# Kernel tuning notes

Measured on AMD Instinct MI355X. Metric: run time of the kernel, lower is better.

## Reference

```python
import jax, jax.numpy as jnp
import numpy as np

D_MODEL = 14
N_HEADS = 2
SINK_TEMP = 0.1
SINK_ITERS = 20
EPS = 1e-10


def setup_inputs() -> dict:
    key = jax.random.key(0)
    ks = jax.random.split(key, 12)
    b, n, d = 64, 1024, D_MODEL
    s = 1.0 / np.sqrt(d)
    return {
        "x": jax.random.normal(ks[0], (b, n, d), dtype=jnp.float32),
        "certainty": jax.random.uniform(ks[1], (b, n), dtype=jnp.float32),
        "permutation": jax.random.randint(ks[2], (b, n), 0, n).astype(jnp.int64),
        "Wq": jax.random.normal(ks[3], (d, d), dtype=jnp.float32) * s,
        "bq": jnp.zeros((d,), dtype=jnp.float32),
        "Wk": jax.random.normal(ks[4], (d, d), dtype=jnp.float32) * s,
        "bk": jnp.zeros((d,), dtype=jnp.float32),
        "Wv": jax.random.normal(ks[5], (d, d), dtype=jnp.float32) * s,
        "bv": jnp.zeros((d,), dtype=jnp.float32),
        "Wo": jax.random.normal(ks[6], (d, d), dtype=jnp.float32) * s,
        "bo": jnp.zeros((d,), dtype=jnp.float32),
    }


def _split_heads(t, b, n):
    # (b, n, d) -> (b, H, n, hd)
    return t.reshape(b, n, N_HEADS, D_MODEL // N_HEADS).transpose(0, 2, 1, 3)


def reference(x, certainty, permutation, Wq, bq, Wk, bk, Wv, bv, Wo, bo):
    b, n, d = x.shape
    hd = d // N_HEADS
    Q = _split_heads(x @ Wq.T + bq, b, n)
    K = _split_heads(x @ Wk.T + bk, b, n)
    V = _split_heads(x @ Wv.T + bv, b, n)
    scores = jnp.einsum("bhqd,bhkd->bhqk", Q, K) / jnp.sqrt(jnp.float32(hd))
    attn = jax.nn.softmax(scores, axis=-1)  # dropout is identity at eval
    out = jnp.einsum("bhqk,bhkd->bhqd", attn, V)
    out = out.transpose(0, 2, 1, 3).reshape(b, n, d)
    out = out @ Wo.T + bo

    avg_attn = attn.mean(axis=1)  # (b, n, n)
    entropy = -jnp.sum(avg_attn * jnp.log(avg_attn + EPS), axis=-1)  # (b, n)
    max_entropy = jnp.log(jnp.float32(n))
    cert_update = jax.nn.sigmoid(max_entropy - entropy)
    new_certainty = jnp.maximum(certainty, cert_update)

    logits = jnp.log(avg_attn + EPS)
    P = jnp.exp(logits / SINK_TEMP)

    def body(_, P):
        P = P / (P.sum(axis=-1, keepdims=True) + EPS)
        P = P / (P.sum(axis=-2, keepdims=True) + EPS)
        return P

    P = jax.lax.fori_loop(0, SINK_ITERS, body, P)
    new_perm = jnp.argmax(P, axis=-1)  # (b, n)
    new_permutation = jnp.take_along_axis(permutation, new_perm, axis=1)
    return out, new_certainty, new_permutation
```

## Files before the change

### kernel.cpp

```cpp
#include <hip/hip_runtime.h>

#define EPSF    1e-10f
#define MAXENT  6.93147180559945286f
#define SCALEF  0.37796447300922720f

__device__ __forceinline__ float wave_sum(float v) {
#pragma unroll
  for (int off = 32; off > 0; off >>= 1) v += __shfl_xor(v, off);
  return v;
}
__device__ __forceinline__ void wave_sum2(float& a, float& b) {
#pragma unroll
  for (int off = 32; off > 0; off >>= 1) {
    a += __shfl_xor(a, off);
    b += __shfl_xor(b, off);
  }
}
__device__ __forceinline__ void fma4(float a, float4 b, float4& c) {
  c.x = fmaf(a, b.x, c.x); c.y = fmaf(a, b.y, c.y);
  c.z = fmaf(a, b.z, c.z); c.w = fmaf(a, b.w, c.w);
}
__device__ __forceinline__ float dot4(float4 a, float4 b, float acc) {
  acc = fmaf(a.x, b.x, acc); acc = fmaf(a.y, b.y, acc);
  acc = fmaf(a.z, b.z, acc); acc = fmaf(a.w, b.w, acc);
  return acc;
}
__device__ __forceinline__ float exp4sum(float4 s) {
  return __expf(s.x) + __expf(s.y) + __expf(s.z) + __expf(s.w);
}
__device__ __forceinline__ float p0e(float s1, float s2, float E1, float E2) {
  float p = fmaf(E1, __expf(s1), fmaf(E2, __expf(s2), EPSF));
  float p2 = p * p, p4 = p2 * p2, p5 = p4 * p;
  return p5 * p5;
}

__global__ __launch_bounds__(256) void qkv_kernel(
    const float* __restrict__ x,
    const float* __restrict__ Wq, const float* __restrict__ bq,
    const float* __restrict__ Wk, const float* __restrict__ bk,
    const float* __restrict__ Wv, const float* __restrict__ bv,
    float* __restrict__ Qt, float* __restrict__ Kt, float* __restrict__ Vt,
    float* __restrict__ R, float* __restrict__ CA, float* __restrict__ CB) {
  int row = blockIdx.x * 256 + threadIdx.x;
  int b = row >> 10, i = row & 1023;
  float xv[14];
#pragma unroll
  for (int k = 0; k < 14; k++) xv[k] = x[row * 14 + k];
#pragma unroll
  for (int d = 0; d < 14; d++) {
    float q = bq[d], kk = bk[d], vv = bv[d];
#pragma unroll
    for (int k = 0; k < 14; k++) {
      q  = fmaf(xv[k], Wq[d * 14 + k], q);
      kk = fmaf(xv[k], Wk[d * 14 + k], kk);
      vv = fmaf(xv[k], Wv[d * 14 + k], vv);
    }
    int o = b * 14336 + d * 1024 + i;
    Qt[o] = q * SCALEF;
    Kt[o] = kk; Vt[o] = vv;
  }
  R[row] = 1.0f;
  CA[row] = 1.0f;
  CB[row] = 1.0f;
}

__global__ __launch_bounds__(512) void attn_kernel(
    const float* __restrict__ Qt, const float* __restrict__ Kt, const float* __restrict__ Vt,
    const float* __restrict__ cert_in,
    float* __restrict__ E1o, float* __restrict__ E2o,
    float* __restrict__ attn_o, float* __restrict__ cert_out) {
  __shared__ float4 Kl[3584];
  int b = blockIdx.x >> 6;
  int rg = blockIdx.x & 63;
  int tid = threadIdx.x;
  const float4* Ktb = (const float4*)(Kt + b * 14336);
  for (int idx = tid; idx < 3584; idx += 512) Kl[idx] = Ktb[idx];
  __syncthreads();

  int wave = tid >> 6, lane = tid & 63;
  int i0 = rg * 16 + wave * 2;
  float q0[14], q1[14];
#pragma unroll
  for (int d = 0; d < 14; d++) {
    q0[d] = Qt[b * 14336 + d * 1024 + i0];
    q1[d] = Qt[b * 14336 + d * 1024 + i0 + 1];
  }

  float L10 = 0.f, L20 = 0.f, L11 = 0.f, L21 = 0.f;
#pragma unroll
  for (int t = 0; t < 4; t++) {
    int g = t * 64 + lane;
    float4 kv[7];
#pragma unroll
    for (int d = 0; d < 7; d++) kv[d] = Kl[d * 256 + g];
    float4 sa = {0,0,0,0}, sb = {0,0,0,0};
#pragma unroll
    for (int d = 0; d < 7; d++) { fma4(q0[d], kv[d], sa); fma4(q1[d], kv[d], sb); }
    L10 += exp4sum(sa); L11 += exp4sum(sb);
#pragma unroll
    for (int d = 0; d < 7; d++) kv[d] = Kl[(d + 7) * 256 + g];
    sa = make_float4(0,0,0,0); sb = make_float4(0,0,0,0);
#pragma unroll
    for (int d = 0; d < 7; d++) { fma4(q0[d + 7], kv[d], sa); fma4(q1[d + 7], kv[d], sb); }
    L20 += exp4sum(sa); L21 += exp4sum(sb);
  }
  L10 = wave_sum(L10); L20 = wave_sum(L20);
  L11 = wave_sum(L11); L21 = wave_sum(L21);
  float i10 = 1.0f / L10, i20 = 1.0f / L20, i11 = 1.0f / L11, i21 = 1.0f / L21;

  float acc0[14], acc1[14];
#pragma unroll
  for (int d = 0; d < 14; d++) { acc0[d] = 0.f; acc1[d] = 0.f; }
  float ent0 = 0.f, ent1 = 0.f;
  const float4* Vtb = (const float4*)(Vt + b * 14336);
#pragma unroll
  for (int t = 0; t < 4; t++) {
    int g = t * 64 + lane;
    float4 kv[7];
#pragma unroll
    for (int d = 0; d < 7; d++) kv[d] = Kl[d * 256 + g];
    float4 sa = {0,0,0,0}, sb = {0,0,0,0};
#pragma unroll
    for (int d = 0; d < 7; d++) { fma4(q0[d], kv[d], sa); fma4(q1[d], kv[d], sb); }
    float4 e10 = make_float4(__expf(sa.x), __expf(sa.y), __expf(sa.z), __expf(sa.w));
    float4 e11 = make_float4(__expf(sb.x), __expf(sb.y), __expf(sb.z), __expf(sb.w));
#pragma unroll
    for (int d = 0; d < 7; d++) kv[d] = Kl[(d + 7) * 256 + g];
    sa = make_float4(0,0,0,0); sb = make_float4(0,0,0,0);
#pragma unroll
    for (int d = 0; d < 7; d++) { fma4(q0[d + 7], kv[d], sa); fma4(q1[d + 7], kv[d], sb); }
    float4 e20 = make_float4(__expf(sa.x), __expf(sa.y), __expf(sa.z), __expf(sa.w));
    float4 e21 = make_float4(__expf(sb.x), __expf(sb.y), __expf(sb.z), __expf(sb.w));
#pragma unroll
    for (int d = 0; d < 7; d++) {
      float4 vv = Vtb[d * 256 + g];
      acc0[d] += e10.x * vv.x + e10.y * vv.y + e10.z * vv.z + e10.w * vv.w;
      acc1[d] += e11.x * vv.x + e11.y * vv.y + e11.z * vv.z + e11.w * vv.w;
    }
#pragma unroll
    for (int d = 7; d < 14; d++) {
      float4 vv = Vtb[d * 256 + g];
      acc0[d] += e20.x * vv.x + e20.y * vv.y + e20.z * vv.z + e20.w * vv.w;
      acc1[d] += e21.x * vv.x + e21.y * vv.y + e21.z * vv.z + e21.w * vv.w;
    }
    float a;
    a = 0.5f * (e10.x * i10 + e20.x * i20); ent0 -= a * __logf(a + EPSF);
    a = 0.5f * (e10.y * i10 + e20.y * i20); ent0 -= a * __logf(a + EPSF);
    a = 0.5f * (e10.z * i10 + e20.z * i20); ent0 -= a * __logf(a + EPSF);
    a = 0.5f * (e10.w * i10 + e20.w * i20); ent0 -= a * __logf(a + EPSF);
    a = 0.5f * (e11.x * i11 + e21.x * i21); ent1 -= a * __logf(a + EPSF);
    a = 0.5f * (e11.y * i11 + e21.y * i21); ent1 -= a * __logf(a + EPSF);
    a = 0.5f * (e11.z * i11 + e21.z * i21); ent1 -= a * __logf(a + EPSF);
    a = 0.5f * (e11.w * i11 + e21.w * i21); ent1 -= a * __logf(a + EPSF);
  }
  ent0 = wave_sum(ent0); ent1 = wave_sum(ent1);
#pragma unroll
  for (int d = 0; d < 14; d++) { acc0[d] = wave_sum(acc0[d]); acc1[d] = wave_sum(acc1[d]); }

  if (lane == 0) {
    int row0 = b * 1024 + i0;
    E1o[row0] = 0.5f * i10;  E2o[row0] = 0.5f * i20;
    E1o[row0 + 1] = 0.5f * i11; E2o[row0 + 1] = 0.5f * i21;
#pragma unroll
    for (int d = 0; d < 14; d++) {
      attn_o[row0 * 14 + d] = acc0[d] * (d < 7 ? i10 : i20);
      attn_o[(row0 + 1) * 14 + d] = acc1[d] * (d < 7 ? i11 : i21);
    }
    cert_out[row0] = fmaxf(cert_in[row0], 1.0f / (1.0f + __expf(ent0 - MAXENT)));
    cert_out[row0 + 1] = fmaxf(cert_in[row0 + 1], 1.0f / (1.0f + __expf(ent1 - MAXENT)));
  }
}

__global__ __launch_bounds__(256) void proj_kernel(
    const float* __restrict__ attn_o, const float* __restrict__ Wo,
    const float* __restrict__ bo, float* __restrict__ out) {
  int idx = blockIdx.x * 256 + threadIdx.x;
  if (idx >= 917504) return;
  int row = idx / 14, d = idx - row * 14;
  float s = bo[d];
  const float* ar = attn_o + row * 14;
  const float* wr = Wo + d * 14;
#pragma unroll
  for (int k = 0; k < 14; k++) s = fmaf(ar[k], wr[k], s);
  out[idx] = s;
}


__global__ __launch_bounds__(512) void p0pre_kernel(
    const float* __restrict__ Qt, const float* __restrict__ Kt,
    const float* __restrict__ E1, const float* __restrict__ E2,
    float* __restrict__ P0, int b0) {
  __shared__ float4 Kl[3584];
  int gb = blockIdx.x >> 5, blk = blockIdx.x & 31;
  int b = b0 + gb;
  int tid = threadIdx.x;
  const float4* Ktb = (const float4*)(Kt + b * 14336);
  for (int idx = tid; idx < 3584; idx += 512) Kl[idx] = Ktb[idx];
  __syncthreads();

  int wave = tid >> 6, lane = tid & 63;
  int i0 = blk * 32 + wave * 4;
  float q[4][14], e1r[4], e2r[4];
#pragma unroll
  for (int rr = 0; rr < 4; rr++) {
#pragma unroll
    for (int d = 0; d < 14; d++) q[rr][d] = Qt[b * 14336 + d * 1024 + i0 + rr];
    e1r[rr] = E1[b * 1024 + i0 + rr];
    e2r[rr] = E2[b * 1024 + i0 + rr];
  }
  float4* P0f4 = (float4*)P0;
#pragma unroll
  for (int t = 0; t < 4; t++) {
    int g = t * 64 + lane;
    float4 kv[14];
#pragma unroll
    for (int d = 0; d < 14; d++) kv[d] = Kl[d * 256 + g];
#pragma unroll
    for (int rr = 0; rr < 4; rr++) {
      float4 s1 = {0,0,0,0}, s2 = {0,0,0,0};
#pragma unroll
      for (int d = 0; d < 7; d++)  fma4(q[rr][d], kv[d], s1);
#pragma unroll
      for (int d = 7; d < 14; d++) fma4(q[rr][d], kv[d], s2);
      float4 pv;
      pv.x = p0e(s1.x, s2.x, e1r[rr], e2r[rr]);
      pv.y = p0e(s1.y, s2.y, e1r[rr], e2r[rr]);
      pv.z = p0e(s1.z, s2.z, e1r[rr], e2r[rr]);
      pv.w = p0e(s1.w, s2.w, e1r[rr], e2r[rr]);
      P0f4[(size_t)(gb * 1024 + i0 + rr) * 256 + g] = pv;
    }
  }
}

#define SINK_LOGS 4
#define SINK_S    16
__global__ __launch_bounds__(512) void sink_fused(
    const float* __restrict__ P0, const float* __restrict__ Cin,
    float* __restrict__ Cout, float* __restrict__ R,
    const float* __restrict__ vprev, float* __restrict__ vcur,
    int b0, int G) {
  __shared__ float Cl[1024];
  __shared__ float vbuf[8192];
  int tid = threadIdx.x;
  int gb = blockIdx.x >> SINK_LOGS, slice = blockIdx.x & (SINK_S - 1);
  int b = b0 + gb;

  for (int col = tid; col < 1024; col += 512) {
    float cv = Cin[b * 1024 + col];
    if (vprev) {
      const float* vp = vprev + gb * 1024 + col;
      float v = 0.f;
#pragma unroll
      for (int s = 0; s < SINK_S; s++) v += vp[(size_t)s * G * 1024];
      cv = fminf(cv / fmaf(cv, v, EPSF), 1e37f);
      if (slice == 0) Cout[b * 1024 + col] = cv;
    }
    Cl[col] = cv;
  }
  __syncthreads();

  int wave = tid >> 6, lane = tid & 63;
  int i0 = slice * 64 + wave * 8;
  int rbase = b * 1024 + i0;
  int l0 = lane, l1 = 64 + lane, l2 = 128 + lane, l3 = 192 + lane;
  const float4* Cl4 = (const float4*)Cl;
  float4 c0 = Cl4[l0], c1 = Cl4[l1], c2 = Cl4[l2], c3 = Cl4[l3];
  float4 v0 = {0,0,0,0}, v1 = {0,0,0,0}, v2 = {0,0,0,0}, v3 = {0,0,0,0};
  const float4* base = (const float4*)P0 + (size_t)(gb * 1024 + i0) * 256;

  float rreg[8];
#pragma unroll
  for (int r = 0; r < 8; r++) rreg[r] = R[rbase + r];

  float4 a0 = base[l0], a1 = base[l1], a2 = base[l2], a3 = base[l3];
  float4 b0f = base[256 + l0], b1f = base[256 + l1], b2f = base[256 + l2], b3f = base[256 + l3];

#pragma unroll
  for (int r = 0; r < 8; r += 2) {
    float4 na0, na1, na2, na3, nb0, nb1, nb2, nb3;
    if (r + 2 < 8) {
      const float4* nxt = base + (r + 2) * 256;
      na0 = nxt[l0]; na1 = nxt[l1]; na2 = nxt[l2]; na3 = nxt[l3];
      nb0 = nxt[256 + l0]; nb1 = nxt[256 + l1]; nb2 = nxt[256 + l2]; nb3 = nxt[256 + l3];
    }
    float ua = dot4(a3, c3, dot4(a2, c2, dot4(a1, c1, dot4(a0, c0, 0.f))));
    float ub = dot4(b3f, c3, dot4(b2f, c2, dot4(b1f, c1, dot4(b0f, c0, 0.f))));
    wave_sum2(ua, ub);
    float rva = rreg[r], rvb = rreg[r + 1];
    rva = fminf(rva / fmaf(rva, ua, EPSF), 1e37f);
    rvb = fminf(rvb / fmaf(rvb, ub, EPSF), 1e37f);
    if (lane == 0) { R[rbase + r] = rva; R[rbase + r + 1] = rvb; }
    fma4(rva, a0, v0); fma4(rva, a1, v1); fma4(rva, a2, v2); fma4(rva, a3, v3);
    fma4(rvb, b0f, v0); fma4(rvb, b1f, v1); fma4(rvb, b2f, v2); fma4(rvb, b3f, v3);
    if (r + 2 < 8) {
      a0 = na0; a1 = na1; a2 = na2; a3 = na3;
      b0f = nb0; b1f = nb1; b2f = nb2; b3f = nb3;
    }
  }
  float4* vb4 = (float4*)vbuf;
  vb4[wave * 256 + l0] = v0; vb4[wave * 256 + l1] = v1;
  vb4[wave * 256 + l2] = v2; vb4[wave * 256 + l3] = v3;
  __syncthreads();
  for (int col = tid; col < 1024; col += 512) {
    float v = 0.f;
#pragma unroll
    for (int w = 0; w < 8; w++) v += vbuf[w * 1024 + col];
    vcur[(size_t)(slice * G + gb) * 1024 + col] = v;
  }
}

__global__ __launch_bounds__(256) void cfinal_kernel(
    const float* __restrict__ Cin, float* __restrict__ Cfin,
    const float* __restrict__ vprev, int b0, int G) {
  int idx = blockIdx.x * 256 + threadIdx.x;
  int gb = idx >> 10, col = idx & 1023;
  const float* vp = vprev + gb * 1024 + col;
  float v = 0.f;
#pragma unroll
  for (int s = 0; s < SINK_S; s++) v += vp[(size_t)s * G * 1024];
  int o = (b0 + gb) * 1024 + col;
  float cv = Cin[o];
  Cfin[o] = fminf(cv / fmaf(cv, v, EPSF), 1e37f);
}

__global__ __launch_bounds__(512) void argmaxP_kernel(
    const float* __restrict__ P0, const float* __restrict__ Cg,
    const int* __restrict__ perm, float* __restrict__ perm_out, int b0) {
  int gb = blockIdx.x >> 7, rg = blockIdx.x & 127;
  int b = b0 + gb;
  int tid = threadIdx.x;
  int wave = tid >> 6, lane = tid & 63;
  int i = rg * 8 + wave;
  const float4* Cb = (const float4*)(Cg + b * 1024);
  const float4* Prow = (const float4*)P0 + (size_t)(gb * 1024 + i) * 256;

  float best = -1.0f;
  int bj = 0;
#pragma unroll
  for (int t = 0; t < 4; t++) {
    int g = t * 64 + lane;
    float4 pv = Prow[g], cv = Cb[g];
    float val;
    val = pv.x * cv.x; if (val > best) { best = val; bj = 4 * g + 0; }
    val = pv.y * cv.y; if (val > best) { best = val; bj = 4 * g + 1; }
    val = pv.z * cv.z; if (val > best) { best = val; bj = 4 * g + 2; }
    val = pv.w * cv.w; if (val > best) { best = val; bj = 4 * g + 3; }
  }
#pragma unroll
  for (int off = 32; off > 0; off >>= 1) {
    float ob = __shfl_xor(best, off);
    int oj = __shfl_xor(bj, off);
    if (ob > best || (ob == best && oj < bj)) { best = ob; bj = oj; }
  }
  if (lane == 0) perm_out[b * 1024 + i] = (float)perm[b * 1024 + bj];
}


__global__ __launch_bounds__(512) void sinkA_kernel(
    const float* __restrict__ Qt, const float* __restrict__ Kt,
    const float* __restrict__ E1, const float* __restrict__ E2,
    const float* __restrict__ C, float* __restrict__ R) {
  __shared__ float4 Kl[3584];
  int b = blockIdx.x >> 5, blk = blockIdx.x & 31;
  int tid = threadIdx.x;
  const float4* Ktb = (const float4*)(Kt + b * 14336);
  for (int idx = tid; idx < 3584; idx += 512) Kl[idx] = Ktb[idx];
  __syncthreads();
  int wave = tid >> 6, lane = tid & 63;
  int i0 = blk * 32 + wave * 4;
  float q[4][14], e1r[4], e2r[4], u[4];
#pragma unroll
  for (int rr = 0; rr < 4; rr++) {
#pragma unroll
    for (int d = 0; d < 14; d++) q[rr][d] = Qt[b * 14336 + d * 1024 + i0 + rr];
    e1r[rr] = E1[b * 1024 + i0 + rr];
    e2r[rr] = E2[b * 1024 + i0 + rr];
    u[rr] = 0.f;
  }
  const float4* Cb = (const float4*)(C + b * 1024);
#pragma unroll
  for (int t = 0; t < 4; t++) {
    int g = t * 64 + lane;
    float4 kv[14];
#pragma unroll
    for (int d = 0; d < 14; d++) kv[d] = Kl[d * 256 + g];
    float4 cv = Cb[g];
#pragma unroll
    for (int rr = 0; rr < 4; rr++) {
      float4 s1 = {0,0,0,0}, s2 = {0,0,0,0};
#pragma unroll
      for (int d = 0; d < 7; d++)  fma4(q[rr][d], kv[d], s1);
#pragma unroll
      for (int d = 7; d < 14; d++) fma4(q[rr][d], kv[d], s2);
      u[rr] += p0e(s1.x, s2.x, e1r[rr], e2r[rr]) * cv.x;
      u[rr] += p0e(s1.y, s2.y, e1r[rr], e2r[rr]) * cv.y;
      u[rr] += p0e(s1.z, s2.z, e1r[rr], e2r[rr]) * cv.z;
      u[rr] += p0e(s1.w, s2.w, e1r[rr], e2r[rr]) * cv.w;
    }
  }
#pragma unroll
  for (int rr = 0; rr < 4; rr++) u[rr] = wave_sum(u[rr]);
  if (lane == 0) {
#pragma unroll
    for (int rr = 0; rr < 4; rr++) {
      int o = b * 1024 + i0 + rr;
      float rv = R[o];
      R[o] = fminf(rv / fmaf(rv, u[rr], EPSF), 1e37f);
    }
  }
}

__global__ __launch_bounds__(512) void sinkB_kernel(
    const float* __restrict__ Qt, const float* __restrict__ Kt,
    const float* __restrict__ E1, const float* __restrict__ E2,
    const float* __restrict__ R, float* __restrict__ C) {
  __shared__ float4 Ql[3584];
  int b = blockIdx.x >> 5, blk = blockIdx.x & 31;
  int tid = threadIdx.x;
  const float4* Qtb = (const float4*)(Qt + b * 14336);
  for (int idx = tid; idx < 3584; idx += 512) Ql[idx] = Qtb[idx];
  __syncthreads();
  int wave = tid >> 6, lane = tid & 63;
  int j0 = blk * 32 + wave * 4;
  float kk[4][14], v[4];
#pragma unroll
  for (int rr = 0; rr < 4; rr++) {
#pragma unroll
    for (int d = 0; d < 14; d++) kk[rr][d] = Kt[b * 14336 + d * 1024 + j0 + rr];
    v[rr] = 0.f;
  }
  const float4* E1b = (const float4*)(E1 + b * 1024);
  const float4* E2b = (const float4*)(E2 + b * 1024);
  const float4* Rb  = (const float4*)(R + b * 1024);
#pragma unroll
  for (int t = 0; t < 4; t++) {
    int g = t * 64 + lane;
    float4 qv[14];
#pragma unroll
    for (int d = 0; d < 14; d++) qv[d] = Ql[d * 256 + g];
    float4 e1v = E1b[g], e2v = E2b[g], rv = Rb[g];
#pragma unroll
    for (int rr = 0; rr < 4; rr++) {
      float4 s1 = {0,0,0,0}, s2 = {0,0,0,0};
#pragma unroll
      for (int d = 0; d < 7; d++)  fma4(kk[rr][d], qv[d], s1);
#pragma unroll
      for (int d = 7; d < 14; d++) fma4(kk[rr][d], qv[d], s2);
      v[rr] += p0e(s1.x, s2.x, e1v.x, e2v.x) * rv.x;
      v[rr] += p0e(s1.y, s2.y, e1v.y, e2v.y) * rv.y;
      v[rr] += p0e(s1.z, s2.z, e1v.z, e2v.z) * rv.z;
      v[rr] += p0e(s1.w, s2.w, e1v.w, e2v.w) * rv.w;
    }
  }
#pragma unroll
  for (int rr = 0; rr < 4; rr++) v[rr] = wave_sum(v[rr]);
  if (lane == 0) {
#pragma unroll
    for (int rr = 0; rr < 4; rr++) {
      int o = b * 1024 + j0 + rr;
      float cv = C[o];
      C[o] = fminf(cv / fmaf(cv, v[rr], EPSF), 1e37f);
    }
  }
}

__global__ __launch_bounds__(512) void argmax_kernel(
    const float* __restrict__ Qt, const float* __restrict__ Kt,
    const float* __restrict__ E1, const float* __restrict__ E2,
    const float* __restrict__ C, const int* __restrict__ perm,
    float* __restrict__ perm_out) {
  __shared__ float4 Kl[3584];
  int b = blockIdx.x >> 7, rg = blockIdx.x & 127;
  int tid = threadIdx.x;
  const float4* Ktb = (const float4*)(Kt + b * 14336);
  for (int idx = tid; idx < 3584; idx += 512) Kl[idx] = Ktb[idx];
  __syncthreads();
  int wave = tid >> 6, lane = tid & 63;
  int i = rg * 8 + wave;
  int row = b * 1024 + i;
  float q[14];
#pragma unroll
  for (int d = 0; d < 14; d++) q[d] = Qt[b * 14336 + d * 1024 + i];
  float e1r = E1[row], e2r = E2[row];
  const float4* Cb = (const float4*)(C + b * 1024);
  float best = -1.0f;
  int bj = 0;
#pragma unroll
  for (int t = 0; t < 4; t++) {
    int g = t * 64 + lane;
    float4 kv[14];
#pragma unroll
    for (int d = 0; d < 14; d++) kv[d] = Kl[d * 256 + g];
    float4 cv = Cb[g];
    float4 s1 = {0,0,0,0}, s2 = {0,0,0,0};
#pragma unroll
    for (int d = 0; d < 7; d++)  fma4(q[d], kv[d], s1);
#pragma unroll
    for (int d = 7; d < 14; d++) fma4(q[d], kv[d], s2);
    float val;
    val = p0e(s1.x, s2.x, e1r, e2r) * cv.x; if (val > best) { best = val; bj = 4 * g + 0; }
    val = p0e(s1.y, s2.y, e1r, e2r) * cv.y; if (val > best) { best = val; bj = 4 * g + 1; }
    val = p0e(s1.z, s2.z, e1r, e2r) * cv.z; if (val > best) { best = val; bj = 4 * g + 2; }
    val = p0e(s1.w, s2.w, e1r, e2r) * cv.w; if (val > best) { best = val; bj = 4 * g + 3; }
  }
#pragma unroll
  for (int off = 32; off > 0; off >>= 1) {
    float ob = __shfl_xor(best, off);
    int oj = __shfl_xor(bj, off);
    if (ob > best || (ob == best && oj < bj)) { best = ob; bj = oj; }
  }
  if (lane == 0) perm_out[row] = (float)perm[b * 1024 + bj];
}

extern "C" void kernel_launch(void* const* d_in, const int* in_sizes, int n_in,
                              void* d_out, int out_size, void* d_ws, size_t ws_size,
                              hipStream_t stream) {
  const float* x    = (const float*)d_in[0];
  const float* cert = (const float*)d_in[1];
  const int*   perm = (const int*)d_in[2];
  const float* Wq = (const float*)d_in[3];
  const float* bq = (const float*)d_in[4];
  const float* Wk = (const float*)d_in[5];
  const float* bk = (const float*)d_in[6];
  const float* Wv = (const float*)d_in[7];
  const float* bv = (const float*)d_in[8];
  const float* Wo = (const float*)d_in[9];
  const float* bo = (const float*)d_in[10];

  float* out      = (float*)d_out;
  float* cert_out = out + 917504;
  float* perm_out = out + 983040;

  float* ws = (float*)d_ws;
  float* Qt = ws;
  float* Kt = Qt + 917504;
  float* Vt = Kt + 917504;
  float* E1 = Vt + 917504;
  float* E2 = E1 + 65536;
  float* R  = E2 + 65536;
  float* CA = R + 65536;
  float* CB = CA + 65536;
  float* attn_o = CB + 65536;
  float* vpp0   = attn_o + 917504;

  size_t base_f = 3997696u;
  size_t avail_f = (ws_size / 4 > base_f) ? (ws_size / 4 - base_f) : 0;
  int G = 0;
  if (avail_f >= (size_t)64 * (32768 + 1048576)) G = 64;
  else if (avail_f >= (size_t)32 * (32768 + 1048576)) G = 32;
  else if (avail_f >= (size_t)16 * (32768 + 1048576)) G = 16;

  float* Cbuf[2] = {CA, CB};

  qkv_kernel<<<256, 256, 0, stream>>>(x, Wq, bq, Wk, bk, Wv, bv, Qt, Kt, Vt, R, CA, CB);
  attn_kernel<<<4096, 512, 0, stream>>>(Qt, Kt, Vt, cert, E1, E2, attn_o, cert_out);
  proj_kernel<<<3584, 256, 0, stream>>>(attn_o, Wo, bo, out);

  if (G >= 16) {
    float* vpp[2] = {vpp0, vpp0 + (size_t)16 * G * 1024};
    float* P0 = vpp0 + (size_t)32 * G * 1024;
    for (int b0 = 0; b0 < 64; b0 += G) {
      p0pre_kernel<<<G * 32, 512, 0, stream>>>(Qt, Kt, E1, E2, P0, b0);
      for (int it = 1; it <= 20; it++) {
        const float* vprev = (it == 1) ? nullptr : vpp[(it - 1) & 1];
        float* vcur = vpp[it & 1];
        const float* Cin = Cbuf[it & 1];
        float* Cout = Cbuf[(it + 1) & 1];
        sink_fused<<<G * SINK_S, 512, 0, stream>>>(P0, Cin, Cout, R, vprev, vcur, b0, G);
      }
      cfinal_kernel<<<G * 4, 256, 0, stream>>>(Cbuf[1], Cbuf[0], vpp[0], b0, G);
      argmaxP_kernel<<<G * 128, 512, 0, stream>>>(P0, Cbuf[0], perm, perm_out, b0);
    }
  } else {
    for (int it = 0; it < 20; it++) {
      sinkA_kernel<<<2048, 512, 0, stream>>>(Qt, Kt, E1, E2, CA, R);
      sinkB_kernel<<<2048, 512, 0, stream>>>(Qt, Kt, E1, E2, R, CA);
    }
    argmax_kernel<<<8192, 512, 0, stream>>>(Qt, Kt, E1, E2, CA, perm, perm_out);
  }
}
```

Baseline: 1.426 ms.

## Register-block attention rows and split Sinkhorn row sweep into more slices

The attention kernel now handles four query rows per wave instead of two. Each K tile read from LDS and each V load is reused across more rows, and half as many blocks are launched. The fused Sinkhorn kernel uses 32 slices of 32 rows instead of 16 slices of 64 rows, with a launch-bounds occupancy hint, to put more blocks on this memory-bound pass. It also drops the software prefetch of the next row pair. Workspace sizing follows SINK_S. The trade-off is higher register pressure in attention and twice as many partial column-sum vectors to write and reduce in Sinkhorn.

After: 3.093 ms. 2.17x slower.

```diff
diff --git a/kernel.cpp b/kernel.cpp
--- a/kernel.cpp
+++ b/kernel.cpp
@@ -70,104 +70,122 @@
     float* __restrict__ E1o, float* __restrict__ E2o,
     float* __restrict__ attn_o, float* __restrict__ cert_out) {
   __shared__ float4 Kl[3584];
-  int b = blockIdx.x >> 6;
-  int rg = blockIdx.x & 63;
+  int b = blockIdx.x >> 5;
+  int rg = blockIdx.x & 31;
   int tid = threadIdx.x;
   const float4* Ktb = (const float4*)(Kt + b * 14336);
   for (int idx = tid; idx < 3584; idx += 512) Kl[idx] = Ktb[idx];
   __syncthreads();
 
   int wave = tid >> 6, lane = tid & 63;
-  int i0 = rg * 16 + wave * 2;
-  float q0[14], q1[14];
-#pragma unroll
-  for (int d = 0; d < 14; d++) {
-    q0[d] = Qt[b * 14336 + d * 1024 + i0];
-    q1[d] = Qt[b * 14336 + d * 1024 + i0 + 1];
-  }
-
-  float L10 = 0.f, L20 = 0.f, L11 = 0.f, L21 = 0.f;
+  int i0 = rg * 32 + wave * 4;
+  float q[4][14];
+#pragma unroll
+  for (int rr = 0; rr < 4; rr++)
+#pragma unroll
+    for (int d = 0; d < 14; d++) q[rr][d] = Qt[b * 14336 + d * 1024 + i0 + rr];
+
+  float L1[4] = {0, 0, 0, 0}, L2[4] = {0, 0, 0, 0};
 #pragma unroll
   for (int t = 0; t < 4; t++) {
     int g = t * 64 + lane;
     float4 kv[7];
 #pragma unroll
     for (int d = 0; d < 7; d++) kv[d] = Kl[d * 256 + g];
-    float4 sa = {0,0,0,0}, sb = {0,0,0,0};
-#pragma unroll
-    for (int d = 0; d < 7; d++) { fma4(q0[d], kv[d], sa); fma4(q1[d], kv[d], sb); }
-    L10 += exp4sum(sa); L11 += exp4sum(sb);
+#pragma unroll
+    for (int rr = 0; rr < 4; rr++) {
+      float4 s = {0, 0, 0, 0};
+#pragma unroll
+      for (int d = 0; d < 7; d++) fma4(q[rr][d], kv[d], s);
+      L1[rr] += exp4sum(s);
+    }
 #pragma unroll
     for (int d = 0; d < 7; d++) kv[d] = Kl[(d + 7) * 256 + g];
-    sa = make_float4(0,0,0,0); sb = make_float4(0,0,0,0);
-#pragma unroll
-    for (int d = 0; d < 7; d++) { fma4(q0[d + 7], kv[d], sa); fma4(q1[d + 7], kv[d], sb); }
-    L20 += exp4sum(sa); L21 += exp4sum(sb);
-  }
-  L10 = wave_sum(L10); L20 = wave_sum(L20);
-  L11 = wave_sum(L11); L21 = wave_sum(L21);
-  float i10 = 1.0f / L10, i20 = 1.0f / L20, i11 = 1.0f / L11, i21 = 1.0f / L21;
-
-  float acc0[14], acc1[14];
-#pragma unroll
-  for (int d = 0; d < 14; d++) { acc0[d] = 0.f; acc1[d] = 0.f; }
-  float ent0 = 0.f, ent1 = 0.f;
+#pragma unroll
+    for (int rr = 0; rr < 4; rr++) {
+      float4 s = {0, 0, 0, 0};
+#pragma unroll
+      for (int d = 0; d < 7; d++) fma4(q[rr][d + 7], kv[d], s);
+      L2[rr] += exp4sum(s);
+    }
+  }
+#pragma unroll
+  for (int rr = 0; rr < 4; rr++) wave_sum2(L1[rr], L2[rr]);
+  float i1[4], i2[4];
+#pragma unroll
+  for (int rr = 0; rr < 4; rr++) { i1[rr] = 1.0f / L1[rr]; i2[rr] = 1.0f / L2[rr]; }
+
+  float acc[4][14];
+#pragma unroll
+  for (int rr = 0; rr < 4; rr++)
+#pragma unroll
+    for (int d = 0; d < 14; d++) acc[rr][d] = 0.f;
+  float ent[4] = {0, 0, 0, 0};
   const float4* Vtb = (const float4*)(Vt + b * 14336);
 #pragma unroll
   for (int t = 0; t < 4; t++) {
     int g = t * 64 + lane;
     float4 kv[7];
+    float4 e1[4], e2[4];
 #pragma unroll
     for (int d = 0; d < 7; d++) kv[d] = Kl[d * 256 + g];
-    float4 sa = {0,0,0,0}, sb = {0,0,0,0};
-#pragma unroll
-    for (int d = 0; d < 7; d++) { fma4(q0[d], kv[d], sa); fma4(q1[d], kv[d], sb); }
-    float4 e10 = make_float4(__expf(sa.x), __expf(sa.y), __expf(sa.z), __expf(sa.w));
-    float4 e11 = make_float4(__expf(sb.x), __expf(sb.y), __expf(sb.z), __expf(sb.w));
+#pragma unroll
+    for (int rr = 0; rr < 4; rr++) {
+      float4 s = {0, 0, 0, 0};
+#pragma unroll
+      for (int d = 0; d < 7; d++) fma4(q[rr][d], kv[d], s);
+      e1[rr] = make_float4(__expf(s.x), __expf(s.y), __expf(s.z), __expf(s.w));
+    }
 #pragma unroll
     for (int d = 0; d < 7; d++) kv[d] = Kl[(d + 7) * 256 + g];
-    sa = make_float4(0,0,0,0); sb = make_float4(0,0,0,0);
-#pragma unroll
-    for (int d = 0; d < 7; d++) { fma4(q0[d + 7], kv[d], sa); fma4(q1[d + 7], kv[d], sb); }
-    float4 e20 = make_float4(__expf(sa.x), __expf(sa.y), __expf(sa.z), __expf(sa.w));
-    float4 e21 = make_float4(__expf(sb.x), __expf(sb.y), __expf(sb.z), __expf(sb.w));
+#pragma unroll
+    for (int rr = 0; rr < 4; rr++) {
+      float4 s = {0, 0, 0, 0};
+#pragma unroll
+      for (int d = 0; d < 7; d++) fma4(q[rr][d + 7], kv[d], s);
+      e2[rr] = make_float4(__expf(s.x), __expf(s.y), __expf(s.z), __expf(s.w));
+    }
 #pragma unroll
     for (int d = 0; d < 7; d++) {
       float4 vv = Vtb[d * 256 + g];
-      acc0[d] += e10.x * vv.x + e10.y * vv.y + e10.z * vv.z + e10.w * vv.w;
-      acc1[d] += e11.x * vv.x + e11.y * vv.y + e11.z * vv.z + e11.w * vv.w;
+#pragma unroll
+      for (int rr = 0; rr < 4; rr++)
+        acc[rr][d] += e1[rr].x * vv.x + e1[rr].y * vv.y + e1[rr].z * vv.z + e1[rr].w * vv.w;
     }
 #pragma unroll
     for (int d = 7; d < 14; d++) {
       float4 vv = Vtb[d * 256 + g];
-      acc0[d] += e20.x * vv.x + e20.y * vv.y + e20.z * vv.z + e20.w * vv.w;
-      acc1[d] += e21.x * vv.x + e21.y * vv.y + e21.z * vv.z + e21.w * vv.w;
-    }
-    float a;
-    a = 0.5f * (e10.x * i10 + e20.x * i20); ent0 -= a * __logf(a + EPSF);
-    a = 0.5f * (e10.y * i10 + e20.y * i20); ent0 -= a * __logf(a + EPSF);
-    a = 0.5f * (e10.z * i10 + e20.z * i20); ent0 -= a * __logf(a + EPSF);
-    a = 0.5f * (e10.w * i10 + e20.w * i20); ent0 -= a * __logf(a + EPSF);
-    a = 0.5f * (e11.x * i11 + e21.x * i21); ent1 -= a * __logf(a + EPSF);
-    a = 0.5f * (e11.y * i11 + e21.y * i21); ent1 -= a * __logf(a + EPSF);
-    a = 0.5f * (e11.z * i11 + e21.z * i21); ent1 -= a * __logf(a + EPSF);
-    a = 0.5f * (e11.w * i11 + e21.w * i21); ent1 -= a * __logf(a + EPSF);
-  }
-  ent0 = wave_sum(ent0); ent1 = wave_sum(ent1);
-#pragma unroll
-  for (int d = 0; d < 14; d++) { acc0[d] = wave_sum(acc0[d]); acc1[d] = wave_sum(acc1[d]); }
+#pragma unroll
+      for (int rr = 0; rr < 4; rr++)
+        acc[rr][d] += e2[rr].x * vv.x + e2[rr].y * vv.y + e2[rr].z * vv.z + e2[rr].w * vv.w;
+    }
+#pragma unroll
+    for (int rr = 0; rr < 4; rr++) {
+      float a;
+      a = 0.5f * (e1[rr].x * i1[rr] + e2[rr].x * i2[rr]); ent[rr] -= a * __logf(a + EPSF);
+      a = 0.5f * (e1[rr].y * i1[rr] + e2[rr].y * i2[rr]); ent[rr] -= a * __logf(a + EPSF);
+      a = 0.5f * (e1[rr].z * i1[rr] + e2[rr].z * i2[rr]); ent[rr] -= a * __logf(a + EPSF);
+      a = 0.5f * (e1[rr].w * i1[rr] + e2[rr].w * i2[rr]); ent[rr] -= a * __logf(a + EPSF);
+    }
+  }
+#pragma unroll
+  for (int rr = 0; rr < 4; rr += 2) wave_sum2(ent[rr], ent[rr + 1]);
+#pragma unroll
+  for (int rr = 0; rr < 4; rr++)
+#pragma unroll
+    for (int d = 0; d < 14; d += 2) wave_sum2(acc[rr][d], acc[rr][d + 1]);
 
   if (lane == 0) {
-    int row0 = b * 1024 + i0;
-    E1o[row0] = 0.5f * i10;  E2o[row0] = 0.5f * i20;
-    E1o[row0 + 1] = 0.5f * i11; E2o[row0 + 1] = 0.5f * i21;
-#pragma unroll
-    for (int d = 0; d < 14; d++) {
-      attn_o[row0 * 14 + d] = acc0[d] * (d < 7 ? i10 : i20);
-      attn_o[(row0 + 1) * 14 + d] = acc1[d] * (d < 7 ? i11 : i21);
-    }
-    cert_out[row0] = fmaxf(cert_in[row0], 1.0f / (1.0f + __expf(ent0 - MAXENT)));
-    cert_out[row0 + 1] = fmaxf(cert_in[row0 + 1], 1.0f / (1.0f + __expf(ent1 - MAXENT)));
+#pragma unroll
+    for (int rr = 0; rr < 4; rr++) {
+      int row = b * 1024 + i0 + rr;
+      E1o[row] = 0.5f * i1[rr];
+      E2o[row] = 0.5f * i2[rr];
+#pragma unroll
+      for (int d = 0; d < 14; d++)
+        attn_o[row * 14 + d] = acc[rr][d] * (d < 7 ? i1[rr] : i2[rr]);
+      cert_out[row] = fmaxf(cert_in[row], 1.0f / (1.0f + __expf(ent[rr] - MAXENT)));
+    }
   }
 }
 
@@ -232,9 +250,9 @@
   }
 }
 
-#define SINK_LOGS 4
-#define SINK_S    16
-__global__ __launch_bounds__(512) void sink_fused(
+#define SINK_LOGS 5
+#define SINK_S    32
+__global__ __launch_bounds__(512, 6) void sink_fused(
     const float* __restrict__ P0, const float* __restrict__ Cin,
     float* __restrict__ Cout, float* __restrict__ R,
     const float* __restrict__ vprev, float* __restrict__ vcur,
@@ -260,7 +278,7 @@
   __syncthreads();
 
   int wave = tid >> 6, lane = tid & 63;
-  int i0 = slice * 64 + wave * 8;
+  int i0 = slice * 32 + wave * 4;
   int rbase = b * 1024 + i0;
   int l0 = lane, l1 = 64 + lane, l2 = 128 + lane, l3 = 192 + lane;
   const float4* Cl4 = (const float4*)Cl;
@@ -268,21 +286,16 @@
   float4 v0 = {0,0,0,0}, v1 = {0,0,0,0}, v2 = {0,0,0,0}, v3 = {0,0,0,0};
   const float4* base = (const float4*)P0 + (size_t)(gb * 1024 + i0) * 256;
 
-  float rreg[8];
-#pragma unroll
-  for (int r = 0; r < 8; r++) rreg[r] = R[rbase + r];
-
-  float4 a0 = base[l0], a1 = base[l1], a2 = base[l2], a3 = base[l3];
-  float4 b0f = base[256 + l0], b1f = base[256 + l1], b2f = base[256 + l2], b3f = base[256 + l3];
-
-#pragma unroll
-  for (int r = 0; r < 8; r += 2) {
-    float4 na0, na1, na2, na3, nb0, nb1, nb2, nb3;
-    if (r + 2 < 8) {
-      const float4* nxt = base + (r + 2) * 256;
-      na0 = nxt[l0]; na1 = nxt[l1]; na2 = nxt[l2]; na3 = nxt[l3];
-      nb0 = nxt[256 + l0]; nb1 = nxt[256 + l1]; nb2 = nxt[256 + l2]; nb3 = nxt[256 + l3];
-    }
+  float rreg[4];
+#pragma unroll
+  for (int r = 0; r < 4; r++) rreg[r] = R[rbase + r];
+
+#pragma unroll
+  for (int r = 0; r < 4; r += 2) {
+    const float4* rowA = base + r * 256;
+    const float4* rowB = rowA + 256;
+    float4 a0 = rowA[l0], a1 = rowA[l1], a2 = rowA[l2], a3 = rowA[l3];
+    float4 b0f = rowB[l0], b1f = rowB[l1], b2f = rowB[l2], b3f = rowB[l3];
     float ua = dot4(a3, c3, dot4(a2, c2, dot4(a1, c1, dot4(a0, c0, 0.f))));
     float ub = dot4(b3f, c3, dot4(b2f, c2, dot4(b1f, c1, dot4(b0f, c0, 0.f))));
     wave_sum2(ua, ub);
@@ -292,10 +305,6 @@
     if (lane == 0) { R[rbase + r] = rva; R[rbase + r + 1] = rvb; }
     fma4(rva, a0, v0); fma4(rva, a1, v1); fma4(rva, a2, v2); fma4(rva, a3, v3);
     fma4(rvb, b0f, v0); fma4(rvb, b1f, v1); fma4(rvb, b2f, v2); fma4(rvb, b3f, v3);
-    if (r + 2 < 8) {
-      a0 = na0; a1 = na1; a2 = na2; a3 = na3;
-      b0f = nb0; b1f = nb1; b2f = nb2; b3f = nb3;
-    }
   }
   float4* vb4 = (float4*)vbuf;
   vb4[wave * 256 + l0] = v0; vb4[wave * 256 + l1] = v1;
@@ -545,20 +554,21 @@
 
   size_t base_f = 3997696u;
   size_t avail_f = (ws_size / 4 > base_f) ? (ws_size / 4 - base_f) : 0;
+  size_t perG = 2u * SINK_S * 1024 + 1048576u;
   int G = 0;
-  if (avail_f >= (size_t)64 * (32768 + 1048576)) G = 64;
-  else if (avail_f >= (size_t)32 * (32768 + 1048576)) G = 32;
-  else if (avail_f >= (size_t)16 * (32768 + 1048576)) G = 16;
+  if (avail_f >= 64 * perG) G = 64;
+  else if (avail_f >= 32 * perG) G = 32;
+  else if (avail_f >= 16 * perG) G = 16;
 
   float* Cbuf[2] = {CA, CB};
 
   qkv_kernel<<<256, 256, 0, stream>>>(x, Wq, bq, Wk, bk, Wv, bv, Qt, Kt, Vt, R, CA, CB);
-  attn_kernel<<<4096, 512, 0, stream>>>(Qt, Kt, Vt, cert, E1, E2, attn_o, cert_out);
+  attn_kernel<<<2048, 512, 0, stream>>>(Qt, Kt, Vt, cert, E1, E2, attn_o, cert_out);
   proj_kernel<<<3584, 256, 0, stream>>>(attn_o, Wo, bo, out);
 
   if (G >= 16) {
-    float* vpp[2] = {vpp0, vpp0 + (size_t)16 * G * 1024};
-    float* P0 = vpp0 + (size_t)32 * G * 1024;
+    float* vpp[2] = {vpp0, vpp0 + (size_t)SINK_S * G * 1024};
+    float* P0 = vpp0 + (size_t)2 * SINK_S * G * 1024;
     for (int b0 = 0; b0 < 64; b0 += G) {
       p0pre_kernel<<<G * 32, 512, 0, stream>>>(Qt, Kt, E1, E2, P0, b0);
       for (int it = 1; it <= 20; it++) {
```

## Fuse first Sinkhorn iteration into P0 precompute kernel

Applied to the files above, without the earlier changes.

The P0 precompute kernel now also does the first Sinkhorn row normalization and writes column partial sums, which removes one sink_fused launch and one full pass over P0. It reads back the P0 rows it just wrote (likely still in cache) to build the column partials, writing 32 partial slices instead of 16, so the next iteration's reduction reads more data. The column-scale update in sink_fused is also vectorized to float4 over 256 threads, and the workspace layout is enlarged to hold the wider partial buffers.

Result: no change. 1.426 ms (-0.0%).

```diff
diff --git a/kernel.cpp b/kernel.cpp
--- a/kernel.cpp
+++ b/kernel.cpp
@@ -186,10 +186,11 @@
 }
 
 
-__global__ __launch_bounds__(512) void p0pre_kernel(
+__global__ __launch_bounds__(512) void p0sink1_kernel(
     const float* __restrict__ Qt, const float* __restrict__ Kt,
     const float* __restrict__ E1, const float* __restrict__ E2,
-    float* __restrict__ P0, int b0) {
+    float* __restrict__ P0, float* __restrict__ R,
+    float* __restrict__ vpart, int b0, int G) {
   __shared__ float4 Kl[3584];
   int gb = blockIdx.x >> 5, blk = blockIdx.x & 31;
   int b = b0 + gb;
@@ -200,13 +201,14 @@
 
   int wave = tid >> 6, lane = tid & 63;
   int i0 = blk * 32 + wave * 4;
-  float q[4][14], e1r[4], e2r[4];
+  float q[4][14], e1r[4], e2r[4], u[4];
 #pragma unroll
   for (int rr = 0; rr < 4; rr++) {
 #pragma unroll
     for (int d = 0; d < 14; d++) q[rr][d] = Qt[b * 14336 + d * 1024 + i0 + rr];
     e1r[rr] = E1[b * 1024 + i0 + rr];
     e2r[rr] = E2[b * 1024 + i0 + rr];
+    u[rr] = 0.f;
   }
   float4* P0f4 = (float4*)P0;
 #pragma unroll
@@ -228,7 +230,40 @@
       pv.z = p0e(s1.z, s2.z, e1r[rr], e2r[rr]);
       pv.w = p0e(s1.w, s2.w, e1r[rr], e2r[rr]);
       P0f4[(size_t)(gb * 1024 + i0 + rr) * 256 + g] = pv;
-    }
+      u[rr] += pv.x; u[rr] += pv.y; u[rr] += pv.z; u[rr] += pv.w;
+    }
+  }
+  wave_sum2(u[0], u[1]); wave_sum2(u[2], u[3]);
+  float rv[4];
+#pragma unroll
+  for (int rr = 0; rr < 4; rr++) {
+    float r0 = 1.0f;
+    rv[rr] = fminf(r0 / fmaf(r0, u[rr], EPSF), 1e37f);
+  }
+  if (lane == 0) {
+#pragma unroll
+    for (int rr = 0; rr < 4; rr++) R[b * 1024 + i0 + rr] = rv[rr];
+  }
+  int l0 = lane, l1 = 64 + lane, l2 = 128 + lane, l3 = 192 + lane;
+  float4 v0 = {0,0,0,0}, v1 = {0,0,0,0}, v2 = {0,0,0,0}, v3 = {0,0,0,0};
+  const float4* base = P0f4 + (size_t)(gb * 1024 + i0) * 256;
+#pragma unroll
+  for (int rr = 0; rr < 4; rr++) {
+    const float4* row = base + rr * 256;
+    float4 a0 = row[l0], a1 = row[l1], a2 = row[l2], a3 = row[l3];
+    fma4(rv[rr], a0, v0); fma4(rv[rr], a1, v1); fma4(rv[rr], a2, v2); fma4(rv[rr], a3, v3);
+  }
+  __syncthreads();
+  float* vbuf = (float*)Kl;
+  float4* vb4 = (float4*)vbuf;
+  vb4[wave * 256 + l0] = v0; vb4[wave * 256 + l1] = v1;
+  vb4[wave * 256 + l2] = v2; vb4[wave * 256 + l3] = v3;
+  __syncthreads();
+  for (int col = tid; col < 1024; col += 512) {
+    float v = 0.f;
+#pragma unroll
+    for (int w = 0; w < 8; w++) v += vbuf[w * 1024 + col];
+    vpart[(size_t)(blk * G + gb) * 1024 + col] = v;
   }
 }
 
@@ -238,24 +273,28 @@
     const float* __restrict__ P0, const float* __restrict__ Cin,
     float* __restrict__ Cout, float* __restrict__ R,
     const float* __restrict__ vprev, float* __restrict__ vcur,
-    int b0, int G) {
+    int b0, int G, int Sprev) {
   __shared__ float Cl[1024];
   __shared__ float vbuf[8192];
   int tid = threadIdx.x;
   int gb = blockIdx.x >> SINK_LOGS, slice = blockIdx.x & (SINK_S - 1);
   int b = b0 + gb;
 
-  for (int col = tid; col < 1024; col += 512) {
-    float cv = Cin[b * 1024 + col];
-    if (vprev) {
-      const float* vp = vprev + gb * 1024 + col;
-      float v = 0.f;
-#pragma unroll
-      for (int s = 0; s < SINK_S; s++) v += vp[(size_t)s * G * 1024];
-      cv = fminf(cv / fmaf(cv, v, EPSF), 1e37f);
-      if (slice == 0) Cout[b * 1024 + col] = cv;
-    }
-    Cl[col] = cv;
+  if (tid < 256) {
+    float4 cv = ((const float4*)(Cin + b * 1024))[tid];
+    const float4* vp = (const float4*)vprev + (size_t)gb * 256 + tid;
+    float4 v = {0, 0, 0, 0};
+#pragma unroll 4
+    for (int s = 0; s < Sprev; s++) {
+      float4 t = vp[(size_t)s * G * 256];
+      v.x += t.x; v.y += t.y; v.z += t.z; v.w += t.w;
+    }
+    cv.x = fminf(cv.x / fmaf(cv.x, v.x, EPSF), 1e37f);
+    cv.y = fminf(cv.y / fmaf(cv.y, v.y, EPSF), 1e37f);
+    cv.z = fminf(cv.z / fmaf(cv.z, v.z, EPSF), 1e37f);
+    cv.w = fminf(cv.w / fmaf(cv.w, v.w, EPSF), 1e37f);
+    if (slice == 0) ((float4*)(Cout + b * 1024))[tid] = cv;
+    ((float4*)Cl)[tid] = cv;
   }
   __syncthreads();
 
@@ -545,10 +584,11 @@
 
   size_t base_f = 3997696u;
   size_t avail_f = (ws_size / 4 > base_f) ? (ws_size / 4 - base_f) : 0;
+  size_t perG = 2u * 32 * 1024 + 1048576u;
   int G = 0;
-  if (avail_f >= (size_t)64 * (32768 + 1048576)) G = 64;
-  else if (avail_f >= (size_t)32 * (32768 + 1048576)) G = 32;
-  else if (avail_f >= (size_t)16 * (32768 + 1048576)) G = 16;
+  if (avail_f >= 64 * perG) G = 64;
+  else if (avail_f >= 32 * perG) G = 32;
+  else if (avail_f >= 16 * perG) G = 16;
 
   float* Cbuf[2] = {CA, CB};
 
@@ -557,16 +597,17 @@
   proj_kernel<<<3584, 256, 0, stream>>>(attn_o, Wo, bo, out);
 
   if (G >= 16) {
-    float* vpp[2] = {vpp0, vpp0 + (size_t)16 * G * 1024};
-    float* P0 = vpp0 + (size_t)32 * G * 1024;
+    float* vpp[2] = {vpp0, vpp0 + (size_t)32 * G * 1024};
+    float* P0 = vpp0 + (size_t)2 * 32 * G * 1024;
     for (int b0 = 0; b0 < 64; b0 += G) {
-      p0pre_kernel<<<G * 32, 512, 0, stream>>>(Qt, Kt, E1, E2, P0, b0);
-      for (int it = 1; it <= 20; it++) {
-        const float* vprev = (it == 1) ? nullptr : vpp[(it - 1) & 1];
+      p0sink1_kernel<<<G * 32, 512, 0, stream>>>(Qt, Kt, E1, E2, P0, R, vpp[1], b0, G);
+      for (int it = 2; it <= 20; it++) {
+        const float* vprev = vpp[(it - 1) & 1];
         float* vcur = vpp[it & 1];
         const float* Cin = Cbuf[it & 1];
         float* Cout = Cbuf[(it + 1) & 1];
-        sink_fused<<<G * SINK_S, 512, 0, stream>>>(P0, Cin, Cout, R, vprev, vcur, b0, G);
+        int Sprev = (it == 2) ? 32 : 16;
+        sink_fused<<<G * SINK_S, 512, 0, stream>>>(P0, Cin, Cout, R, vprev, vcur, b0, G, Sprev);
       }
       cfinal_kernel<<<G * 4, 256, 0, stream>>>(Cbuf[1], Cbuf[0], vpp[0], b0, G);
       argmaxP_kernel<<<G * 128, 512, 0, stream>>>(P0, Cbuf[0], perm, perm_out, b0);
```
